# Optimization experiments

Measured on AMD Instinct MI355X. Metric: run time of the kernel, lower is better.

Reference implementation:

```python
import jax, jax.numpy as jnp
import numpy as np

B, TM1, D, H = 1024, 255, 128, 128  # batch, n_timestep-1, input_size, hidden_size


def setup_inputs() -> dict:
    key = jax.random.key(0)
    ks = jax.random.split(key, 7)
    s = 0.05
    return {
        "input_data": jax.random.normal(ks[0], (B, TM1, D), jnp.float32),
        "Wa": jax.random.normal(ks[1], (1, 2 * H + TM1), jnp.float32) * s,
        "ba": jax.random.normal(ks[2], (1,), jnp.float32) * s,
        "W_ih": jax.random.normal(ks[3], (4 * H, D), jnp.float32) * s,
        "W_hh": jax.random.normal(ks[4], (4 * H, H), jnp.float32) * s,
        "b_ih": jax.random.normal(ks[5], (4 * H,), jnp.float32) * s,
        "b_hh": jax.random.normal(ks[6], (4 * H,), jnp.float32) * s,
    }


def _encoder(input_data, Wa, ba, W_ih, W_hh, b_ih, b_hh):
    b, tm1, d = input_data.shape
    h_dim = W_hh.shape[1]
    # Split attention weight into hidden / cell / time-series parts.
    Wh, Wc, Wx = Wa[0, :h_dim], Wa[0, h_dim:2 * h_dim], Wa[0, 2 * h_dim:]
    # Contribution of the (constant across steps) full driving series: (B, D)
    x_part = jnp.einsum("btd,t->bd", input_data, Wx)

    def step(carry, x_t):  # x_t: (B, D) = input_data[:, t, :]
        h, c = carry  # each (B, H)
        # attn score[b, d] = Wh.h[b] + Wc.c[b] + Wx.x[b, :, d] + ba  -> (B, D)
        score = x_part + (h @ Wh)[:, None] + (c @ Wc)[:, None] + ba[0]
        attn = jax.nn.softmax(score, axis=1)
        wx = attn * x_t  # weighted input (B, D)
        # single LSTM cell step, PyTorch gate order i, f, g, o
        gates = wx @ W_ih.T + b_ih + h @ W_hh.T + b_hh  # (B, 4H)
        i, f, g, o = jnp.split(gates, 4, axis=1)
        c_new = jax.nn.sigmoid(f) * c + jax.nn.sigmoid(i) * jnp.tanh(g)
        h_new = jax.nn.sigmoid(o) * jnp.tanh(c_new)
        return (h_new, c_new), (wx, h_new)

    h0 = jnp.zeros((b, h_dim), input_data.dtype)
    c0 = jnp.zeros((b, h_dim), input_data.dtype)
    xs = jnp.transpose(input_data, (1, 0, 2))  # (T-1, B, D)
    _, (wts, enc) = jax.lax.scan(step, (h0, c0), xs)
    input_weighted = jnp.transpose(wts, (1, 0, 2))  # (B, T-1, D)
    input_encoded = jnp.transpose(enc, (1, 0, 2))   # (B, T-1, H)
    return input_weighted, input_encoded


def reference(input_data, Wa, ba, W_ih, W_hh, b_ih, b_hh):
    return _encoder(input_data, Wa, ba, W_ih, W_hh, b_ih, b_hh)
```

## Files before the change

### kernel.cpp

```cpp
#include <hip/hip_runtime.h>
#include <hip/hip_bf16.h>
#include <stdint.h>

#define B_ 1024
#define T_ 255
#define D_ 128

typedef float f32x4 __attribute__((ext_vector_type(4)));
typedef short s16x8 __attribute__((ext_vector_type(8)));
typedef unsigned u32x4 __attribute__((ext_vector_type(4)));

__device__ __forceinline__ unsigned pk2(float a, float b){
  __hip_bfloat162 h2 = __float22bfloat162_rn(make_float2(a, b));
  union { __hip_bfloat162 h; unsigned u; } c; c.h = h2; return c.u;
}
__device__ __forceinline__ unsigned short bf1(float a){
  __hip_bfloat16 h = __float2bfloat16(a);
  union { __hip_bfloat16 h; unsigned short u; } c; c.h = h; return c.u;
}
__device__ __forceinline__ float sigm_f(float x){
  return __builtin_amdgcn_rcpf(1.f + __expf(-x));
}
__device__ __forceinline__ float tanh_f2(float x){
  return fmaf(-2.f, __builtin_amdgcn_rcpf(1.f + __expf(2.f * x)), 1.f);
}

__global__ __launch_bounds__(512) void k_attn(const float* __restrict__ x,
    const float* __restrict__ Wa, float* __restrict__ out_w,
    uint2* __restrict__ wxq){
  extern __shared__ float4 xs4[];
  __shared__ float wxs[256];
  __shared__ float part_s[16][128];
  __shared__ float red[128];
  __shared__ float attn_s[128];
  int tid = threadIdx.x, b = blockIdx.x;
  if (tid < T_) wxs[tid] = Wa[2 * D_ + tid];
  __syncthreads();
  const float4* xg = (const float4*)(x + (size_t)b * T_ * D_);
  float4 acc = {0.f, 0.f, 0.f, 0.f};
  for (int i = tid; i < 8160; i += 512){
    float4 v = xg[i];
    xs4[i] = v;
    float wt = wxs[i >> 5];
    acc.x += v.x * wt; acc.y += v.y * wt; acc.z += v.z * wt; acc.w += v.w * wt;
  }
  int d0 = (tid & 31) * 4, s = tid >> 5;
  *(float4*)&part_s[s][d0] = acc;
  __syncthreads();
  if (tid < 128){
    float v = 0.f;
    #pragma unroll
    for (int k = 0; k < 16; k++) v += part_s[k][tid];
    red[tid] = v; attn_s[tid] = v;
  }
  __syncthreads();
  for (int st = 64; st >= 1; st >>= 1){
    if (tid < st) red[tid] = fmaxf(red[tid], red[tid + st]);
    __syncthreads();
  }
  float mx = red[0];
  __syncthreads();
  float ev = 0.f;
  if (tid < 128){ ev = __expf(attn_s[tid] - mx); red[tid] = ev; }
  __syncthreads();
  for (int st = 64; st >= 1; st >>= 1){
    if (tid < st) red[tid] += red[tid + st];
    __syncthreads();
  }
  float sm = red[0];
  if (tid < 128) attn_s[tid] = ev / sm;
  __syncthreads();
  float4 at = *(const float4*)&attn_s[d0];
  float4* owg = (float4*)(out_w + (size_t)b * T_ * D_);
  for (int i = tid; i < 8160; i += 512){
    float4 v = xs4[i];
    float4 wv; wv.x = v.x*at.x; wv.y = v.y*at.y; wv.z = v.z*at.z; wv.w = v.w*at.w;
    owg[i] = wv;
    int t = i >> 5;
    uint2 q;
    q.x = pk2(wv.x, wv.y);
    q.y = pk2(wv.z, wv.w);
    wxq[((size_t)t * B_ + b) * 32 + (i & 31)] = q;
  }
}

__global__ __launch_bounds__(512, 2) void k_rnn(const float* __restrict__ W_ih,
    const float* __restrict__ W_hh, const float* __restrict__ b_ih,
    const float* __restrict__ b_hh, const unsigned short* __restrict__ wxb,
    float* __restrict__ out_e){
  __shared__ char hl[2048];
  __shared__ float4 g1l[2048];
  int tid = threadIdx.x;
  int lane = tid & 63, w = tid >> 6;
  int l15 = lane & 15, lg = lane >> 4;
  int row0 = blockIdx.x << 2;
  int d = w * 16 + l15;
  int hr = l15 >> 2;

  s16x8 fih[4][4], fhh[4][4];
  float bias[4];
  #pragma unroll
  for (int g = 0; g < 4; g++){
    int n = g * 128 + w * 16 + l15;
    bias[g] = b_ih[n] + b_hh[n];
    #pragma unroll
    for (int kt = 0; kt < 4; kt++){
      const float4* p1 = (const float4*)(W_ih + n * D_ + kt * 32 + lg * 8);
      float4 a0 = p1[0], a1 = p1[1];
      u32x4 bv;
      bv[0] = pk2(a0.x, a0.y); bv[1] = pk2(a0.z, a0.w);
      bv[2] = pk2(a1.x, a1.y); bv[3] = pk2(a1.z, a1.w);
      fih[kt][g] = __builtin_bit_cast(s16x8, bv);
      const float4* p2 = (const float4*)(W_hh + n * D_ + kt * 32 + lg * 8);
      float4 c0v = p2[0], c1v = p2[1];
      u32x4 cv;
      cv[0] = pk2(c0v.x, c0v.y); cv[1] = pk2(c0v.z, c0v.w);
      cv[2] = pk2(c1v.x, c1v.y); cv[3] = pk2(c1v.z, c1v.w);
      fhh[kt][g] = __builtin_bit_cast(s16x8, cv);
    }
  }
  unsigned rd_[4];
  #pragma unroll
  for (int kt = 0; kt < 4; kt++)
    rd_[kt] = (unsigned)(hr * 256 + (((kt << 2) + lg) ^ ((hr & 1) << 2)) * 16);
  unsigned wr_ = (unsigned)(lg * 256 + ((d >> 3) ^ ((lg & 1) << 2)) * 16 + (d & 7) * 2);

  float* op = out_e + (size_t)(row0 + lg) * T_ * D_ + d;
  float cst = 0.f;
  if (tid < 128) ((uint2*)hl)[tid] = make_uint2(0u, 0u);

  int gw0 = lg * 512 + d;
  int gr0 = lg * 128 + d;

  const unsigned short* wp = wxb + ((size_t)(l15 >> 2) * B_ + row0 + (l15 & 3)) * D_ + lg * 8;
  const size_t GSTRIDE = (size_t)4 * B_ * D_;
  s16x8 AF[4];
  #pragma unroll
  for (int kt = 0; kt < 4; kt++) AF[kt] = *(const s16x8*)(wp + kt * 32);
  wp += GSTRIDE;
  __syncthreads();

#define FIH_BATCH() do {                                                            \
    f32x4 bi = {bias[0], bias[0], bias[0], bias[0]};                                \
    f32x4 bf = {bias[1], bias[1], bias[1], bias[1]};                                \
    f32x4 bg = {bias[2], bias[2], bias[2], bias[2]};                                \
    f32x4 bo = {bias[3], bias[3], bias[3], bias[3]};                                \
    _Pragma("unroll")                                                               \
    for (int kt = 0; kt < 4; kt++){                                                 \
      bi = __builtin_amdgcn_mfma_f32_16x16x32_bf16(AF[kt], fih[kt][0], bi,0,0,0);   \
      bf = __builtin_amdgcn_mfma_f32_16x16x32_bf16(AF[kt], fih[kt][1], bf,0,0,0);   \
      bg = __builtin_amdgcn_mfma_f32_16x16x32_bf16(AF[kt], fih[kt][2], bg,0,0,0);   \
      bo = __builtin_amdgcn_mfma_f32_16x16x32_bf16(AF[kt], fih[kt][3], bo,0,0,0);   \
    }                                                                               \
    _Pragma("unroll")                                                               \
    for (int r = 0; r < 4; r++)                                                     \
      g1l[gw0 + r * 128] = make_float4(bi[r], bf[r], bg[r], bo[r]);                 \
  } while (0)

#define STEP(TS) do {                                                               \
    s16x8 aa[4];                                                                    \
    _Pragma("unroll")                                                               \
    for (int kt = 0; kt < 4; kt++)                                                  \
      aa[kt] = *(const s16x8*)(hl + rd_[kt] + ((TS) & 1) * 1024);                   \
    f32x4 a0 = {0.f,0.f,0.f,0.f}, a1 = a0, a2 = a0, a3 = a0;                        \
    _Pragma("unroll")                                                               \
    for (int kt = 0; kt < 4; kt++){                                                 \
      a0 = __builtin_amdgcn_mfma_f32_16x16x32_bf16(aa[kt], fhh[kt][0], a0,0,0,0);   \
      a1 = __builtin_amdgcn_mfma_f32_16x16x32_bf16(aa[kt], fhh[kt][1], a1,0,0,0);   \
      a2 = __builtin_amdgcn_mfma_f32_16x16x32_bf16(aa[kt], fhh[kt][2], a2,0,0,0);   \
      a3 = __builtin_amdgcn_mfma_f32_16x16x32_bf16(aa[kt], fhh[kt][3], a3,0,0,0);   \
    }                                                                               \
    float4 q = g1l[gr0 + (TS) * 512];                                               \
    float gi = q.x + a0[0], gf = q.y + a1[0];                                       \
    float gg = q.z + a2[0], go = q.w + a3[0];                                       \
    float cn = fmaf(sigm_f(gf), cst, sigm_f(gi) * tanh_f2(gg));                     \
    float hn = sigm_f(go) * tanh_f2(cn); cst = cn;                                  \
    *op = hn; op += D_;                                                             \
    *(unsigned short*)(hl + wr_ + (1 - ((TS) & 1)) * 1024) = bf1(hn);               \
    __syncthreads();                                                                \
  } while (0)

  for (int g = 0; g < 63; g++){
    FIH_BATCH();
    #pragma unroll
    for (int kt = 0; kt < 4; kt++) AF[kt] = *(const s16x8*)(wp + kt * 32);
    wp += GSTRIDE;
    STEP(0); STEP(1); STEP(2); STEP(3);
  }
  FIH_BATCH();
  STEP(0); STEP(1); STEP(2);
#undef FIH_BATCH
#undef STEP
}

extern "C" void kernel_launch(void* const* d_in, const int* in_sizes, int n_in,
                              void* d_out, int out_size, void* d_ws, size_t ws_size,
                              hipStream_t stream) {
  (void)in_sizes; (void)n_in; (void)out_size;
  const float* x    = (const float*)d_in[0];
  const float* Wa   = (const float*)d_in[1];
  const float* W_ih = (const float*)d_in[3];
  const float* W_hh = (const float*)d_in[4];
  const float* b_ih = (const float*)d_in[5];
  const float* b_hh = (const float*)d_in[6];
  float* out_w = (float*)d_out;
  float* out_e = out_w + (size_t)B_ * T_ * D_;
  unsigned short* wxb = (unsigned short*)d_ws;
  size_t need = (size_t)(T_ + 1) * B_ * D_ * 2;
  if (ws_size < need) return;

  hipMemsetAsync((char*)d_ws + (size_t)T_ * B_ * D_ * 2, 0, (size_t)B_ * D_ * 2, stream);
  k_attn<<<B_, 512, 130560, stream>>>(x, Wa, out_w, (uint2*)wxb);
  k_rnn <<<256, 512, 0, stream>>>(W_ih, W_hh, b_ih, b_hh, wxb, out_e);
}
```

Before: 234.6 us.

## Double-buffer input-gate fragments and use LDS-only barrier in recurrent steps

```diff
diff --git a/kernel.cpp b/kernel.cpp
--- a/kernel.cpp
+++ b/kernel.cpp
@@ -132,15 +132,21 @@
   int gw0 = lg * 512 + d;
   int gr0 = lg * 128 + d;
 
-  const unsigned short* wp = wxb + ((size_t)(l15 >> 2) * B_ + row0 + (l15 & 3)) * D_ + lg * 8;
+  const unsigned short* wpb = wxb + ((size_t)(l15 >> 2) * B_ + row0 + (l15 & 3)) * D_ + lg * 8;
   const size_t GSTRIDE = (size_t)4 * B_ * D_;
-  s16x8 AF[4];
-  #pragma unroll
-  for (int kt = 0; kt < 4; kt++) AF[kt] = *(const s16x8*)(wp + kt * 32);
-  wp += GSTRIDE;
-  __syncthreads();
-
-#define FIH_BATCH() do {                                                            \
+  s16x8 AF0[4], AF1[4];
+  #pragma unroll
+  for (int kt = 0; kt < 4; kt++) AF0[kt] = *(const s16x8*)(wpb + kt * 32);
+  #pragma unroll
+  for (int kt = 0; kt < 4; kt++) AF1[kt] = *(const s16x8*)(wpb + GSTRIDE + kt * 32);
+  __syncthreads();
+
+#define BAR() do {                                                                  \
+    asm volatile("s_waitcnt lgkmcnt(0)" ::: "memory");                              \
+    __builtin_amdgcn_s_barrier();                                                   \
+  } while (0)
+
+#define FIH_BATCH(AF) do {                                                          \
     f32x4 bi = {bias[0], bias[0], bias[0], bias[0]};                                \
     f32x4 bf = {bias[1], bias[1], bias[1], bias[1]};                                \
     f32x4 bg = {bias[2], bias[2], bias[2], bias[2]};                                \
@@ -177,20 +183,28 @@
     float hn = sigm_f(go) * tanh_f2(cn); cst = cn;                                  \
     *op = hn; op += D_;                                                             \
     *(unsigned short*)(hl + wr_ + (1 - ((TS) & 1)) * 1024) = bf1(hn);               \
-    __syncthreads();                                                                \
+    BAR();                                                                          \
   } while (0)
 
-  for (int g = 0; g < 63; g++){
-    FIH_BATCH();
-    #pragma unroll
-    for (int kt = 0; kt < 4; kt++) AF[kt] = *(const s16x8*)(wp + kt * 32);
-    wp += GSTRIDE;
+  for (int g = 0; g < 62; g += 2){
+    FIH_BATCH(AF0);
+    #pragma unroll
+    for (int kt = 0; kt < 4; kt++)
+      AF0[kt] = *(const s16x8*)(wpb + (size_t)(g + 2) * GSTRIDE + kt * 32);
     STEP(0); STEP(1); STEP(2); STEP(3);
-  }
-  FIH_BATCH();
+    FIH_BATCH(AF1);
+    #pragma unroll
+    for (int kt = 0; kt < 4; kt++)
+      AF1[kt] = *(const s16x8*)(wpb + (size_t)(g + 3) * GSTRIDE + kt * 32);
+    STEP(0); STEP(1); STEP(2); STEP(3);
+  }
+  FIH_BATCH(AF0);
+  STEP(0); STEP(1); STEP(2); STEP(3);
+  FIH_BATCH(AF1);
   STEP(0); STEP(1); STEP(2);
 #undef FIH_BATCH
 #undef STEP
+#undef BAR
 }
 
 extern "C" void kernel_launch(void* const* d_in, const int* in_sizes, int n_in,
```

Measured after the change: 237.5 us. About the same (+1.3%).

## Warp-specialize RNN kernel: separate input-projection waves from recurrent waves

Applied to the files above, without the earlier changes.

```diff
diff --git a/kernel.cpp b/kernel.cpp
--- a/kernel.cpp
+++ b/kernel.cpp
@@ -84,112 +84,131 @@
   }
 }
 
-__global__ __launch_bounds__(512, 2) void k_rnn(const float* __restrict__ W_ih,
+__global__ __launch_bounds__(1024, 4) void k_rnn(const float* __restrict__ W_ih,
     const float* __restrict__ W_hh, const float* __restrict__ b_ih,
     const float* __restrict__ b_hh, const unsigned short* __restrict__ wxb,
     float* __restrict__ out_e){
   __shared__ char hl[2048];
-  __shared__ float4 g1l[2048];
+  __shared__ float4 g1l[4096];
+  __shared__ char wxl[8192];
   int tid = threadIdx.x;
-  int lane = tid & 63, w = tid >> 6;
+  int lane = tid & 63, W = tid >> 6;
   int l15 = lane & 15, lg = lane >> 4;
+  bool isFih = (W >= 8);
+  int w = isFih ? (W - 8) : W;
   int row0 = blockIdx.x << 2;
   int d = w * 16 + l15;
   int hr = l15 >> 2;
 
-  s16x8 fih[4][4], fhh[4][4];
+  const float* Wsrc = isFih ? W_ih : W_hh;
+  s16x8 wfrag[4][4];
   float bias[4];
   #pragma unroll
   for (int g = 0; g < 4; g++){
-    int n = g * 128 + w * 16 + l15;
-    bias[g] = b_ih[n] + b_hh[n];
+    int n = g * 128 + d;
     #pragma unroll
     for (int kt = 0; kt < 4; kt++){
-      const float4* p1 = (const float4*)(W_ih + n * D_ + kt * 32 + lg * 8);
-      float4 a0 = p1[0], a1 = p1[1];
+      const float4* p = (const float4*)(Wsrc + n * D_ + kt * 32 + lg * 8);
+      float4 a0 = p[0], a1 = p[1];
       u32x4 bv;
       bv[0] = pk2(a0.x, a0.y); bv[1] = pk2(a0.z, a0.w);
       bv[2] = pk2(a1.x, a1.y); bv[3] = pk2(a1.z, a1.w);
-      fih[kt][g] = __builtin_bit_cast(s16x8, bv);
-      const float4* p2 = (const float4*)(W_hh + n * D_ + kt * 32 + lg * 8);
-      float4 c0v = p2[0], c1v = p2[1];
-      u32x4 cv;
-      cv[0] = pk2(c0v.x, c0v.y); cv[1] = pk2(c0v.z, c0v.w);
-      cv[2] = pk2(c1v.x, c1v.y); cv[3] = pk2(c1v.z, c1v.w);
-      fhh[kt][g] = __builtin_bit_cast(s16x8, cv);
+      wfrag[kt][g] = __builtin_bit_cast(s16x8, bv);
     }
+    bias[g] = isFih ? (b_ih[n] + b_hh[n]) : 0.f;
   }
   unsigned rd_[4];
   #pragma unroll
   for (int kt = 0; kt < 4; kt++)
     rd_[kt] = (unsigned)(hr * 256 + (((kt << 2) + lg) ^ ((hr & 1) << 2)) * 16);
   unsigned wr_ = (unsigned)(lg * 256 + ((d >> 3) ^ ((lg & 1) << 2)) * 16 + (d & 7) * 2);
-
   float* op = out_e + (size_t)(row0 + lg) * T_ * D_ + d;
   float cst = 0.f;
+  int gr0 = lg * 128 + d;
+  int gw0 = lg * 512 + d;
+
   if (tid < 128) ((uint2*)hl)[tid] = make_uint2(0u, 0u);
 
-  int gw0 = lg * 512 + d;
-  int gr0 = lg * 128 + d;
-
-  const unsigned short* wp = wxb + ((size_t)(l15 >> 2) * B_ + row0 + (l15 & 3)) * D_ + lg * 8;
-  const size_t GSTRIDE = (size_t)4 * B_ * D_;
-  s16x8 AF[4];
-  #pragma unroll
-  for (int kt = 0; kt < 4; kt++) AF[kt] = *(const s16x8*)(wp + kt * 32);
-  wp += GSTRIDE;
-  __syncthreads();
-
-#define FIH_BATCH() do {                                                            \
+#define STAGE(G) do {                                                               \
+    if (w < 4){                                                                     \
+      int u = w * 64 + lane;                                                        \
+      int R = u >> 4, Cl = u & 15;                                                  \
+      const unsigned short* sp = wxb +                                              \
+          ((size_t)((G) * 4 + (R >> 2)) * B_ + row0 + (R & 3)) * D_ + Cl * 8;       \
+      uint4 v = *(const uint4*)sp;                                                  \
+      *(uint4*)(wxl + ((G) & 1) * 4096 + R * 256 + ((Cl ^ (R & 7)) << 4)) = v;      \
+    }                                                                               \
+  } while (0)
+
+#define FIH(G) do {                                                                 \
+    unsigned wsel = ((G) & 1) * 4096;                                               \
+    s16x8 aaA[4];                                                                   \
+    _Pragma("unroll")                                                               \
+    for (int kt = 0; kt < 4; kt++)                                                  \
+      aaA[kt] = *(const s16x8*)(wxl + wsel + l15 * 256 +                            \
+                                ((((kt << 2) + lg) ^ (l15 & 7)) << 4));             \
     f32x4 bi = {bias[0], bias[0], bias[0], bias[0]};                                \
     f32x4 bf = {bias[1], bias[1], bias[1], bias[1]};                                \
     f32x4 bg = {bias[2], bias[2], bias[2], bias[2]};                                \
     f32x4 bo = {bias[3], bias[3], bias[3], bias[3]};                                \
     _Pragma("unroll")                                                               \
     for (int kt = 0; kt < 4; kt++){                                                 \
-      bi = __builtin_amdgcn_mfma_f32_16x16x32_bf16(AF[kt], fih[kt][0], bi,0,0,0);   \
-      bf = __builtin_amdgcn_mfma_f32_16x16x32_bf16(AF[kt], fih[kt][1], bf,0,0,0);   \
-      bg = __builtin_amdgcn_mfma_f32_16x16x32_bf16(AF[kt], fih[kt][2], bg,0,0,0);   \
-      bo = __builtin_amdgcn_mfma_f32_16x16x32_bf16(AF[kt], fih[kt][3], bo,0,0,0);   \
+      bi = __builtin_amdgcn_mfma_f32_16x16x32_bf16(aaA[kt], wfrag[kt][0], bi,0,0,0);\
+      bf = __builtin_amdgcn_mfma_f32_16x16x32_bf16(aaA[kt], wfrag[kt][1], bf,0,0,0);\
+      bg = __builtin_amdgcn_mfma_f32_16x16x32_bf16(aaA[kt], wfrag[kt][2], bg,0,0,0);\
+      bo = __builtin_amdgcn_mfma_f32_16x16x32_bf16(aaA[kt], wfrag[kt][3], bo,0,0,0);\
     }                                                                               \
+    int gsel = ((G) & 1) * 2048;                                                    \
     _Pragma("unroll")                                                               \
     for (int r = 0; r < 4; r++)                                                     \
-      g1l[gw0 + r * 128] = make_float4(bi[r], bf[r], bg[r], bo[r]);                 \
+      g1l[gsel + gw0 + r * 128] = make_float4(bi[r], bf[r], bg[r], bo[r]);          \
   } while (0)
 
-#define STEP(TS) do {                                                               \
-    s16x8 aa[4];                                                                    \
-    _Pragma("unroll")                                                               \
-    for (int kt = 0; kt < 4; kt++)                                                  \
-      aa[kt] = *(const s16x8*)(hl + rd_[kt] + ((TS) & 1) * 1024);                   \
-    f32x4 a0 = {0.f,0.f,0.f,0.f}, a1 = a0, a2 = a0, a3 = a0;                        \
-    _Pragma("unroll")                                                               \
-    for (int kt = 0; kt < 4; kt++){                                                 \
-      a0 = __builtin_amdgcn_mfma_f32_16x16x32_bf16(aa[kt], fhh[kt][0], a0,0,0,0);   \
-      a1 = __builtin_amdgcn_mfma_f32_16x16x32_bf16(aa[kt], fhh[kt][1], a1,0,0,0);   \
-      a2 = __builtin_amdgcn_mfma_f32_16x16x32_bf16(aa[kt], fhh[kt][2], a2,0,0,0);   \
-      a3 = __builtin_amdgcn_mfma_f32_16x16x32_bf16(aa[kt], fhh[kt][3], a3,0,0,0);   \
+#define STEP(TS, GP) do {                                                           \
+    if (!isFih){                                                                    \
+      s16x8 aa[4];                                                                  \
+      _Pragma("unroll")                                                             \
+      for (int kt = 0; kt < 4; kt++)                                                \
+        aa[kt] = *(const s16x8*)(hl + rd_[kt] + ((TS) & 1) * 1024);                 \
+      f32x4 a0 = {0.f,0.f,0.f,0.f}, a1 = a0, a2 = a0, a3 = a0;                      \
+      _Pragma("unroll")                                                             \
+      for (int kt = 0; kt < 4; kt++){                                               \
+        a0 = __builtin_amdgcn_mfma_f32_16x16x32_bf16(aa[kt], wfrag[kt][0], a0,0,0,0);\
+        a1 = __builtin_amdgcn_mfma_f32_16x16x32_bf16(aa[kt], wfrag[kt][1], a1,0,0,0);\
+        a2 = __builtin_amdgcn_mfma_f32_16x16x32_bf16(aa[kt], wfrag[kt][2], a2,0,0,0);\
+        a3 = __builtin_amdgcn_mfma_f32_16x16x32_bf16(aa[kt], wfrag[kt][3], a3,0,0,0);\
+      }                                                                             \
+      float4 q = g1l[(GP) + gr0 + (TS) * 512];                                      \
+      float gi = q.x + a0[0], gf = q.y + a1[0];                                     \
+      float gg = q.z + a2[0], go = q.w + a3[0];                                     \
+      float cn = fmaf(sigm_f(gf), cst, sigm_f(gi) * tanh_f2(gg));                   \
+      float hn = sigm_f(go) * tanh_f2(cn); cst = cn;                                \
+      *op = hn; op += D_;                                                           \
+      *(unsigned short*)(hl + wr_ + (1 - ((TS) & 1)) * 1024) = bf1(hn);             \
     }                                                                               \
-    float4 q = g1l[gr0 + (TS) * 512];                                               \
-    float gi = q.x + a0[0], gf = q.y + a1[0];                                       \
-    float gg = q.z + a2[0], go = q.w + a3[0];                                       \
-    float cn = fmaf(sigm_f(gf), cst, sigm_f(gi) * tanh_f2(gg));                     \
-    float hn = sigm_f(go) * tanh_f2(cn); cst = cn;                                  \
-    *op = hn; op += D_;                                                             \
-    *(unsigned short*)(hl + wr_ + (1 - ((TS) & 1)) * 1024) = bf1(hn);               \
-    __syncthreads();                                                                \
+    asm volatile("s_waitcnt lgkmcnt(0)" ::: "memory");                              \
+    __builtin_amdgcn_s_barrier();                                                   \
   } while (0)
 
-  for (int g = 0; g < 63; g++){
-    FIH_BATCH();
-    #pragma unroll
-    for (int kt = 0; kt < 4; kt++) AF[kt] = *(const s16x8*)(wp + kt * 32);
-    wp += GSTRIDE;
-    STEP(0); STEP(1); STEP(2); STEP(3);
-  }
-  FIH_BATCH();
-  STEP(0); STEP(1); STEP(2);
-#undef FIH_BATCH
+  if (isFih){ STAGE(0); STAGE(1); }
+  __syncthreads();
+  if (isFih) FIH(0);
+  __syncthreads();
+
+  for (int grp = 0; grp < 63; ++grp){
+    if (isFih){
+      FIH(grp + 1);
+      if (grp < 62) STAGE(grp + 2);
+    }
+    int gp = (grp & 1) * 2048;
+    STEP(0, gp); STEP(1, gp); STEP(2, gp); STEP(3, gp);
+  }
+  {
+    int gp = 2048;
+    STEP(0, gp); STEP(1, gp); STEP(2, gp);
+  }
+#undef STAGE
+#undef FIH
 #undef STEP
 }
 
@@ -211,5 +230,5 @@
 
   hipMemsetAsync((char*)d_ws + (size_t)T_ * B_ * D_ * 2, 0, (size_t)B_ * D_ * 2, stream);
   k_attn<<<B_, 512, 130560, stream>>>(x, Wa, out_w, (uint2*)wxb);
-  k_rnn <<<256, 512, 0, stream>>>(W_ih, W_hh, b_ih, b_hh, wxb, out_e);
-}
+  k_rnn <<<256, 1024, 0, stream>>>(W_ih, W_hh, b_ih, b_hh, wxb, out_e);
+}
```

Result: slower. 290.3 us (+23.8%).

## Fuse attention and LSTM recurrence into one kernel with an in-LDS weighted-input ring

Applied to the files above, without the earlier changes.

```diff
diff --git a/kernel.cpp b/kernel.cpp
--- a/kernel.cpp
+++ b/kernel.cpp
@@ -18,104 +18,56 @@
   __hip_bfloat16 h = __float2bfloat16(a);
   union { __hip_bfloat16 h; unsigned short u; } c; c.h = h; return c.u;
 }
-__device__ __forceinline__ float sigm_f(float x){
-  return __builtin_amdgcn_rcpf(1.f + __expf(-x));
-}
-__device__ __forceinline__ float tanh_f2(float x){
-  return fmaf(-2.f, __builtin_amdgcn_rcpf(1.f + __expf(2.f * x)), 1.f);
-}
-
-__global__ __launch_bounds__(512) void k_attn(const float* __restrict__ x,
-    const float* __restrict__ Wa, float* __restrict__ out_w,
-    uint2* __restrict__ wxq){
-  extern __shared__ float4 xs4[];
-  __shared__ float wxs[256];
-  __shared__ float part_s[16][128];
-  __shared__ float red[128];
-  __shared__ float attn_s[128];
-  int tid = threadIdx.x, b = blockIdx.x;
-  if (tid < T_) wxs[tid] = Wa[2 * D_ + tid];
-  __syncthreads();
-  const float4* xg = (const float4*)(x + (size_t)b * T_ * D_);
-  float4 acc = {0.f, 0.f, 0.f, 0.f};
-  for (int i = tid; i < 8160; i += 512){
-    float4 v = xg[i];
-    xs4[i] = v;
-    float wt = wxs[i >> 5];
-    acc.x += v.x * wt; acc.y += v.y * wt; acc.z += v.z * wt; acc.w += v.w * wt;
-  }
-  int d0 = (tid & 31) * 4, s = tid >> 5;
-  *(float4*)&part_s[s][d0] = acc;
-  __syncthreads();
-  if (tid < 128){
-    float v = 0.f;
-    #pragma unroll
-    for (int k = 0; k < 16; k++) v += part_s[k][tid];
-    red[tid] = v; attn_s[tid] = v;
-  }
-  __syncthreads();
-  for (int st = 64; st >= 1; st >>= 1){
-    if (tid < st) red[tid] = fmaxf(red[tid], red[tid + st]);
-    __syncthreads();
-  }
-  float mx = red[0];
-  __syncthreads();
-  float ev = 0.f;
-  if (tid < 128){ ev = __expf(attn_s[tid] - mx); red[tid] = ev; }
-  __syncthreads();
-  for (int st = 64; st >= 1; st >>= 1){
-    if (tid < st) red[tid] += red[tid + st];
-    __syncthreads();
-  }
-  float sm = red[0];
-  if (tid < 128) attn_s[tid] = ev / sm;
-  __syncthreads();
-  float4 at = *(const float4*)&attn_s[d0];
-  float4* owg = (float4*)(out_w + (size_t)b * T_ * D_);
-  for (int i = tid; i < 8160; i += 512){
-    float4 v = xs4[i];
-    float4 wv; wv.x = v.x*at.x; wv.y = v.y*at.y; wv.z = v.z*at.z; wv.w = v.w*at.w;
-    owg[i] = wv;
-    int t = i >> 5;
-    uint2 q;
-    q.x = pk2(wv.x, wv.y);
-    q.y = pk2(wv.z, wv.w);
-    wxq[((size_t)t * B_ + b) * 32 + (i & 31)] = q;
-  }
-}
-
-__global__ __launch_bounds__(512, 2) void k_rnn(const float* __restrict__ W_ih,
+__device__ __forceinline__ float sg(float x){
+  return __builtin_amdgcn_rcpf(1.f + __builtin_amdgcn_exp2f(-x));
+}
+__device__ __forceinline__ float tg(float x){
+  return fmaf(-2.f, __builtin_amdgcn_rcpf(1.f + __builtin_amdgcn_exp2f(x)), 1.f);
+}
+__device__ __forceinline__ float tc_(float c){
+  return fmaf(-2.f, __builtin_amdgcn_rcpf(1.f + __builtin_amdgcn_exp2f(c * 2.88539008f)), 1.f);
+}
+
+__global__ __launch_bounds__(512, 2) void k_fused(const float* __restrict__ x,
+    const float* __restrict__ Wa, const float* __restrict__ W_ih,
     const float* __restrict__ W_hh, const float* __restrict__ b_ih,
-    const float* __restrict__ b_hh, const unsigned short* __restrict__ wxb,
+    const float* __restrict__ b_hh, float* __restrict__ out_w,
     float* __restrict__ out_e){
   __shared__ char hl[2048];
   __shared__ float4 g1l[2048];
+  __shared__ char ring[12672];
+  __shared__ float wxs[256];
+  __shared__ float rbuf[512];
+
   int tid = threadIdx.x;
   int lane = tid & 63, w = tid >> 6;
   int l15 = lane & 15, lg = lane >> 4;
   int row0 = blockIdx.x << 2;
   int d = w * 16 + l15;
   int hr = l15 >> 2;
-
+  int ts = l15 >> 2, br = l15 & 3;
+
+  const float SC0 = 1.44269504f, SC2 = 2.88539008f;
   s16x8 fih[4][4], fhh[4][4];
-  float bias[4];
+  float biasS[4];
   #pragma unroll
   for (int g = 0; g < 4; g++){
-    int n = g * 128 + w * 16 + l15;
-    bias[g] = b_ih[n] + b_hh[n];
+    float sc = (g == 2) ? SC2 : SC0;
+    int n = g * 128 + d;
+    biasS[g] = (b_ih[n] + b_hh[n]) * sc;
     #pragma unroll
     for (int kt = 0; kt < 4; kt++){
       const float4* p1 = (const float4*)(W_ih + n * D_ + kt * 32 + lg * 8);
       float4 a0 = p1[0], a1 = p1[1];
       u32x4 bv;
-      bv[0] = pk2(a0.x, a0.y); bv[1] = pk2(a0.z, a0.w);
-      bv[2] = pk2(a1.x, a1.y); bv[3] = pk2(a1.z, a1.w);
+      bv[0] = pk2(a0.x * sc, a0.y * sc); bv[1] = pk2(a0.z * sc, a0.w * sc);
+      bv[2] = pk2(a1.x * sc, a1.y * sc); bv[3] = pk2(a1.z * sc, a1.w * sc);
       fih[kt][g] = __builtin_bit_cast(s16x8, bv);
       const float4* p2 = (const float4*)(W_hh + n * D_ + kt * 32 + lg * 8);
       float4 c0v = p2[0], c1v = p2[1];
       u32x4 cv;
-      cv[0] = pk2(c0v.x, c0v.y); cv[1] = pk2(c0v.z, c0v.w);
-      cv[2] = pk2(c1v.x, c1v.y); cv[3] = pk2(c1v.z, c1v.w);
+      cv[0] = pk2(c0v.x * sc, c0v.y * sc); cv[1] = pk2(c0v.z * sc, c0v.w * sc);
+      cv[2] = pk2(c1v.x * sc, c1v.y * sc); cv[3] = pk2(c1v.z * sc, c1v.w * sc);
       fhh[kt][g] = __builtin_bit_cast(s16x8, cv);
     }
   }
@@ -124,37 +76,79 @@
   for (int kt = 0; kt < 4; kt++)
     rd_[kt] = (unsigned)(hr * 256 + (((kt << 2) + lg) ^ ((hr & 1) << 2)) * 16);
   unsigned wr_ = (unsigned)(lg * 256 + ((d >> 3) ^ ((lg & 1) << 2)) * 16 + (d & 7) * 2);
-
-  float* op = out_e + (size_t)(row0 + lg) * T_ * D_ + d;
-  float cst = 0.f;
-  if (tid < 128) ((uint2*)hl)[tid] = make_uint2(0u, 0u);
-
   int gw0 = lg * 512 + d;
   int gr0 = lg * 128 + d;
-
-  const unsigned short* wp = wxb + ((size_t)(l15 >> 2) * B_ + row0 + (l15 & 3)) * D_ + lg * 8;
-  const size_t GSTRIDE = (size_t)4 * B_ * D_;
-  s16x8 AF[4];
-  #pragma unroll
-  for (int kt = 0; kt < 4; kt++) AF[kt] = *(const s16x8*)(wp + kt * 32);
-  wp += GSTRIDE;
-  __syncthreads();
-
-#define FIH_BATCH() do {                                                            \
-    f32x4 bi = {bias[0], bias[0], bias[0], bias[0]};                                \
-    f32x4 bf = {bias[1], bias[1], bias[1], bias[1]};                                \
-    f32x4 bg = {bias[2], bias[2], bias[2], bias[2]};                                \
-    f32x4 bo = {bias[3], bias[3], bias[3], bias[3]};                                \
+  unsigned rrd[4];
+  #pragma unroll
+  for (int kt = 0; kt < 4; kt++)
+    rrd[kt] = (unsigned)(ts * 1056 + br * 256 + (((kt << 2) + lg) ^ ((br & 1) << 2)) * 16);
+
+  int prow = tid >> 7, pdq = tid & 127;
+  const float* xrow = x + ((size_t)(row0 + prow) * T_) * D_ + pdq;
+  float* owp = out_w + ((size_t)(row0 + prow) * T_) * D_ + pdq;
+  unsigned wxwr = (unsigned)(prow * 256 + (((pdq >> 3) ^ ((prow & 1) << 2)) << 4) + (pdq & 7) * 2);
+
+  if (tid < T_) wxs[tid] = Wa[2 * D_ + tid];
+  if (tid < 128) ((uint2*)hl)[tid] = make_uint2(0u, 0u);
+  __syncthreads();
+
+  float xp = 0.f;
+  #pragma unroll 5
+  for (int t = 0; t < T_; t++) xp = fmaf(xrow[(size_t)t * D_], wxs[t], xp);
+  rbuf[tid] = xp; __syncthreads();
+  for (int s = 64; s >= 1; s >>= 1){
+    if ((tid & 127) < s) rbuf[tid] = fmaxf(rbuf[tid], rbuf[tid + s]);
+    __syncthreads();
+  }
+  float mx = rbuf[tid & 384];
+  __syncthreads();
+  float ev = __expf(xp - mx);
+  rbuf[tid] = ev; __syncthreads();
+  for (int s = 64; s >= 1; s >>= 1){
+    if ((tid & 127) < s) rbuf[tid] += rbuf[tid + s];
+    __syncthreads();
+  }
+  float attn_own = ev / rbuf[tid & 384];
+  __syncthreads();
+
+  #pragma unroll
+  for (int t = 0; t < 8; t++){
+    float wv = attn_own * xrow[(size_t)t * D_];
+    owp[(size_t)t * D_] = wv;
+    *(unsigned short*)(ring + t * 1056 + wxwr) = bf1(wv);
+  }
+  float xv = xrow[(size_t)8 * D_];
+  float* owp8 = owp + 8 * D_;
+  const float* xl9 = xrow + (size_t)9 * D_;
+  float* op = out_e + ((size_t)(row0 + lg) * T_) * D_ + d;
+  float cst = 0.f;
+  int tcur = 0, t12 = 0;
+  __syncthreads();
+
+#define BAR() do {                                                                  \
+    asm volatile("s_waitcnt lgkmcnt(0)" ::: "memory");                              \
+    __builtin_amdgcn_s_barrier();                                                   \
+  } while (0)
+
+#define FIH(GP3) do {                                                               \
+    s16x8 aaA[4];                                                                   \
+    _Pragma("unroll")                                                               \
+    for (int kt = 0; kt < 4; kt++)                                                  \
+      aaA[kt] = *(const s16x8*)(ring + (GP3) * 4224 + rrd[kt]);                     \
+    f32x4 p0 = {biasS[0], biasS[0], biasS[0], biasS[0]};                            \
+    f32x4 p1 = {biasS[1], biasS[1], biasS[1], biasS[1]};                            \
+    f32x4 p2 = {biasS[2], biasS[2], biasS[2], biasS[2]};                            \
+    f32x4 p3 = {biasS[3], biasS[3], biasS[3], biasS[3]};                            \
     _Pragma("unroll")                                                               \
     for (int kt = 0; kt < 4; kt++){                                                 \
-      bi = __builtin_amdgcn_mfma_f32_16x16x32_bf16(AF[kt], fih[kt][0], bi,0,0,0);   \
-      bf = __builtin_amdgcn_mfma_f32_16x16x32_bf16(AF[kt], fih[kt][1], bf,0,0,0);   \
-      bg = __builtin_amdgcn_mfma_f32_16x16x32_bf16(AF[kt], fih[kt][2], bg,0,0,0);   \
-      bo = __builtin_amdgcn_mfma_f32_16x16x32_bf16(AF[kt], fih[kt][3], bo,0,0,0);   \
+      p0 = __builtin_amdgcn_mfma_f32_16x16x32_bf16(aaA[kt], fih[kt][0], p0,0,0,0);  \
+      p1 = __builtin_amdgcn_mfma_f32_16x16x32_bf16(aaA[kt], fih[kt][1], p1,0,0,0);  \
+      p2 = __builtin_amdgcn_mfma_f32_16x16x32_bf16(aaA[kt], fih[kt][2], p2,0,0,0);  \
+      p3 = __builtin_amdgcn_mfma_f32_16x16x32_bf16(aaA[kt], fih[kt][3], p3,0,0,0);  \
     }                                                                               \
     _Pragma("unroll")                                                               \
     for (int r = 0; r < 4; r++)                                                     \
-      g1l[gw0 + r * 128] = make_float4(bi[r], bf[r], bg[r], bo[r]);                 \
+      g1l[gw0 + r * 128] = make_float4(p0[r], p1[r], p2[r], p3[r]);                 \
   } while (0)
 
 #define STEP(TS) do {                                                               \
@@ -162,7 +156,11 @@
     _Pragma("unroll")                                                               \
     for (int kt = 0; kt < 4; kt++)                                                  \
       aa[kt] = *(const s16x8*)(hl + rd_[kt] + ((TS) & 1) * 1024);                   \
-    f32x4 a0 = {0.f,0.f,0.f,0.f}, a1 = a0, a2 = a0, a3 = a0;                        \
+    float4 q = g1l[gr0 + (TS) * 512];                                               \
+    f32x4 a0 = {q.x, q.x, q.x, q.x};                                                \
+    f32x4 a1 = {q.y, q.y, q.y, q.y};                                                \
+    f32x4 a2 = {q.z, q.z, q.z, q.z};                                                \
+    f32x4 a3 = {q.w, q.w, q.w, q.w};                                                \
     _Pragma("unroll")                                                               \
     for (int kt = 0; kt < 4; kt++){                                                 \
       a0 = __builtin_amdgcn_mfma_f32_16x16x32_bf16(aa[kt], fhh[kt][0], a0,0,0,0);   \
@@ -170,33 +168,39 @@
       a2 = __builtin_amdgcn_mfma_f32_16x16x32_bf16(aa[kt], fhh[kt][2], a2,0,0,0);   \
       a3 = __builtin_amdgcn_mfma_f32_16x16x32_bf16(aa[kt], fhh[kt][3], a3,0,0,0);   \
     }                                                                               \
-    float4 q = g1l[gr0 + (TS) * 512];                                               \
-    float gi = q.x + a0[0], gf = q.y + a1[0];                                       \
-    float gg = q.z + a2[0], go = q.w + a3[0];                                       \
-    float cn = fmaf(sigm_f(gf), cst, sigm_f(gi) * tanh_f2(gg));                     \
-    float hn = sigm_f(go) * tanh_f2(cn); cst = cn;                                  \
+    if (tcur <= 246){                                                               \
+      float wv = attn_own * xv;                                                     \
+      *owp8 = wv; owp8 += D_;                                                       \
+      int ws = (t12 >= 4) ? (t12 - 4) : (t12 + 8);                                  \
+      *(unsigned short*)(ring + ws * 1056 + wxwr) = bf1(wv);                        \
+      if (tcur <= 245){ xv = *xl9; xl9 += D_; }                                     \
+    }                                                                               \
+    tcur++; t12 = (t12 == 11) ? 0 : t12 + 1;                                        \
+    float gi = a0[0], gf = a1[0], gg = a2[0], go = a3[0];                           \
+    float cn = fmaf(sg(gf), cst, sg(gi) * tg(gg));                                  \
+    float hn = sg(go) * tc_(cn); cst = cn;                                          \
     *op = hn; op += D_;                                                             \
     *(unsigned short*)(hl + wr_ + (1 - ((TS) & 1)) * 1024) = bf1(hn);               \
-    __syncthreads();                                                                \
+    BAR();                                                                          \
   } while (0)
 
+  int gp3 = 0;
   for (int g = 0; g < 63; g++){
-    FIH_BATCH();
-    #pragma unroll
-    for (int kt = 0; kt < 4; kt++) AF[kt] = *(const s16x8*)(wp + kt * 32);
-    wp += GSTRIDE;
+    FIH(gp3);
     STEP(0); STEP(1); STEP(2); STEP(3);
-  }
-  FIH_BATCH();
+    gp3 = (gp3 == 2) ? 0 : gp3 + 1;
+  }
+  FIH(gp3);
   STEP(0); STEP(1); STEP(2);
-#undef FIH_BATCH
+#undef FIH
 #undef STEP
+#undef BAR
 }
 
 extern "C" void kernel_launch(void* const* d_in, const int* in_sizes, int n_in,
                               void* d_out, int out_size, void* d_ws, size_t ws_size,
                               hipStream_t stream) {
-  (void)in_sizes; (void)n_in; (void)out_size;
+  (void)in_sizes; (void)n_in; (void)out_size; (void)d_ws; (void)ws_size;
   const float* x    = (const float*)d_in[0];
   const float* Wa   = (const float*)d_in[1];
   const float* W_ih = (const float*)d_in[3];
@@ -205,11 +209,6 @@
   const float* b_hh = (const float*)d_in[6];
   float* out_w = (float*)d_out;
   float* out_e = out_w + (size_t)B_ * T_ * D_;
-  unsigned short* wxb = (unsigned short*)d_ws;
-  size_t need = (size_t)(T_ + 1) * B_ * D_ * 2;
-  if (ws_size < need) return;
-
-  hipMemsetAsync((char*)d_ws + (size_t)T_ * B_ * D_ * 2, 0, (size_t)B_ * D_ * 2, stream);
-  k_attn<<<B_, 512, 130560, stream>>>(x, Wa, out_w, (uint2*)wxb);
-  k_rnn <<<256, 512, 0, stream>>>(W_ih, W_hh, b_ih, b_hh, wxb, out_e);
-}
+
+  k_fused<<<256, 512, 0, stream>>>(x, Wa, W_ih, W_hh, b_ih, b_hh, out_w, out_e);
+}
```

Result: slower. 306.0 us (+30.5%).
